# Optimization experiments

Measured on AMD Instinct MI355X. Metric: run time of the kernel, lower is better.

Reference implementation:

```python
import jax, jax.numpy as jnp
import numpy as np
import math

B, C, FDIM, TP = 32, 64, 128, 32
NHID, NOUT, E, RATIO = 256, 128, 512, 0.8
BN_EPS = 1e-5


def setup_inputs() -> dict:
    key = jax.random.key(0)
    ks = jax.random.split(key, 10)
    nrm = lambda k, shp, s=1.0: jax.random.normal(k, shp, jnp.float32) * s
    return {
        "h": nrm(ks[0], (B, C, FDIM, TP)),
        "edge_index": jax.random.randint(ks[1], (2, E), 0, C, dtype=jnp.int32),
        "edge_weight": jax.random.uniform(ks[2], (E,), jnp.float32),
        "gc1_w": nrm(ks[3], (FDIM, NHID), 1.0 / math.sqrt(FDIM)),
        "gc1_b": jnp.zeros((NHID,), jnp.float32),
        "bn1_gamma": jnp.ones((NHID,), jnp.float32),
        "bn1_beta": jnp.zeros((NHID,), jnp.float32),
        "bn1_mean": jnp.zeros((NHID,), jnp.float32),
        "bn1_var": jnp.ones((NHID,), jnp.float32),
        "prelu1_a": jnp.full((1,), 0.25, jnp.float32),
        "pool1_w": nrm(ks[4], (NHID, 1), 1.0 / math.sqrt(NHID)),
        "pool1_b": jnp.zeros((1,), jnp.float32),
        "gc2_w": nrm(ks[5], (NHID, NOUT), 1.0 / math.sqrt(NHID)),
        "gc2_b": jnp.zeros((NOUT,), jnp.float32),
        "bn2_gamma": jnp.ones((NOUT,), jnp.float32),
        "bn2_beta": jnp.zeros((NOUT,), jnp.float32),
        "bn2_mean": jnp.zeros((NOUT,), jnp.float32),
        "bn2_var": jnp.ones((NOUT,), jnp.float32),
        "prelu2_a": jnp.full((1,), 0.25, jnp.float32),
        "pool2_w": nrm(ks[6], (NOUT, 1), 1.0 / math.sqrt(NOUT)),
        "pool2_b": jnp.zeros((1,), jnp.float32),
    }


def _gcn(x, row, col, w, W, b, n):
    """PyG GCNConv: x @ W, add self-loops (weight 1), symmetric norm, scatter to col, + bias."""
    xw = x @ W
    loop = jnp.arange(n, dtype=row.dtype)
    r = jnp.concatenate([row, loop])
    c = jnp.concatenate([col, loop])
    wf = jnp.concatenate([w, jnp.ones((n,), x.dtype)])
    deg = jax.ops.segment_sum(wf, c, num_segments=n)
    deg_safe = jnp.where(deg > 0, deg, 1.0)
    dis = jnp.where(deg > 0, jax.lax.rsqrt(deg_safe), 0.0)  # deg^-1/2, inf -> 0
    norm = dis[r] * wf * dis[c]
    out = jax.ops.segment_sum(norm[:, None] * xw[r], c, num_segments=n)
    return out + b


def _bn(x, gamma, beta, mean, var):
    return gamma * (x - mean) * jax.lax.rsqrt(var + BN_EPS) + beta


def _prelu(x, a):
    return jnp.where(x >= 0, x, a * x)


def _sagpool(x, row, col, w, valid, Wp, bp, G, N, ratio):
    """SAGPool: GCN score (no edge weights => valid mask as binary weights), per-graph top-k,
    gate by tanh(score), reindex edges (filter_adj via masking). All graphs have N nodes."""
    n = G * N
    score = _gcn(x, row, col, valid.astype(x.dtype), Wp, bp, n)[:, 0]
    k = math.ceil(ratio * N)  # static: uniform graph sizes
    _, idx = jax.lax.top_k(score.reshape(G, N), k)
    perm = (jnp.arange(G, dtype=row.dtype)[:, None] * N + idx.astype(row.dtype)).reshape(-1)
    xk = x[perm] * jnp.tanh(score[perm])[:, None]
    node_map = jnp.full((n,), -1, dtype=row.dtype).at[perm].set(
        jnp.arange(G * k, dtype=row.dtype))
    nr, nc = node_map[row], node_map[col]
    v2 = valid & (nr >= 0) & (nc >= 0)
    nr = jnp.where(v2, nr, 0)
    nc = jnp.where(v2, nc, 0)
    w2 = jnp.where(v2, w, 0.0)
    return xk, nr, nc, w2, v2, k


def _forward(h, edge_index, edge_weight, gc1_w, gc1_b, bn1_gamma, bn1_beta, bn1_mean,
             bn1_var, prelu1_a, pool1_w, pool1_b, gc2_w, gc2_b, bn2_gamma, bn2_beta,
             bn2_mean, bn2_var, prelu2_a, pool2_w, pool2_b):
    b, c, f, tp = h.shape
    G = b * tp
    x = jnp.transpose(h, (0, 3, 1, 2)).reshape(G * c, f)  # fold time into batch of graphs
    offs = jnp.arange(G, dtype=edge_index.dtype) * c
    row = (edge_index[0][None, :] + offs[:, None]).reshape(-1)
    col = (edge_index[1][None, :] + offs[:, None]).reshape(-1)
    w = jnp.tile(edge_weight, G)
    valid = jnp.ones(row.shape, dtype=bool)

    x = _gcn(x, row, col, w, gc1_w, gc1_b, G * c)
    x = _prelu(_bn(x, bn1_gamma, bn1_beta, bn1_mean, bn1_var), prelu1_a)
    x, row, col, w, valid, k1 = _sagpool(x, row, col, w, valid, pool1_w, pool1_b, G, c, RATIO)
    # dropout: eval mode -> identity
    x = _gcn(x, row, col, w, gc2_w, gc2_b, G * k1)
    x = _prelu(_bn(x, bn2_gamma, bn2_beta, bn2_mean, bn2_var), prelu2_a)
    x, row, col, w, valid, k2 = _sagpool(x, row, col, w, valid, pool2_w, pool2_b, G, k1, RATIO)

    z = x.reshape(G, k2, -1).mean(axis=1)  # global_mean_pool (uniform segments)
    z_seq = z.reshape(b, tp, -1)
    return x, z_seq


def reference(h, edge_index, edge_weight, gc1_w, gc1_b, bn1_gamma, bn1_beta, bn1_mean,
              bn1_var, prelu1_a, pool1_w, pool1_b, gc2_w, gc2_b, bn2_gamma, bn2_beta,
              bn2_mean, bn2_var, prelu2_a, pool2_w, pool2_b):
    return _forward(h, edge_index, edge_weight, gc1_w, gc1_b, bn1_gamma, bn1_beta,
                    bn1_mean, bn1_var, prelu1_a, pool1_w, pool1_b, gc2_w, gc2_b,
                    bn2_gamma, bn2_beta, bn2_mean, bn2_var, prelu2_a, pool2_w, pool2_b)
```

## Files before the change

### kernel.cpp

```cpp
#include <hip/hip_runtime.h>
#include <math.h>

#define B_   32
#define C_   64
#define F_   128
#define TP_  32
#define G_   (B_*TP_)
#define NHID 256
#define NOUT 128
#define E_   512
#define K1_  52
#define K2_  42
#define N2_  (G_*K1_)

typedef __attribute__((ext_vector_type(8))) short short8_t;
typedef __attribute__((ext_vector_type(4))) float f32x4_t;

__device__ __forceinline__ void split_bf16(float v, unsigned short &h, unsigned short &l) {
  unsigned u = __float_as_uint(v);
  unsigned hb = (u + 0x7FFFu + ((u >> 16) & 1u)) & 0xFFFF0000u;
  float hf = __uint_as_float(hb);
  float r = v - hf;
  unsigned ur = __float_as_uint(r);
  unsigned lb = (ur + 0x7FFFu + ((ur >> 16) & 1u)) >> 16;
  h = (unsigned short)(hb >> 16);
  l = (unsigned short)lb;
}

__global__ __launch_bounds__(256) void build_A1(const int* __restrict__ ei,
                                                const float* __restrict__ ew,
                                                float* __restrict__ A1,
                                                float* __restrict__ As1) {
  __shared__ float A1s[C_*C_], As1s[C_*C_];
  __shared__ float dg[C_], dgs[C_], dis[C_], diss[C_];
  int t = threadIdx.x;
  for (int i = t; i < C_*C_; i += 256) { A1s[i] = 0.f; As1s[i] = 0.f; }
  if (t < C_) { dg[t] = 1.f; dgs[t] = 1.f; }
  int r0[2], c0[2]; float w0[2];
#pragma unroll
  for (int p = 0; p < 2; ++p) {
    int e = t + p*256;
    r0[p] = ei[e]; c0[p] = ei[E_ + e]; w0[p] = ew[e];
  }
  __syncthreads();
#pragma unroll
  for (int p = 0; p < 2; ++p) {
    atomicAdd(&dg[c0[p]], w0[p]);
    atomicAdd(&dgs[c0[p]], 1.f);
  }
  __syncthreads();
  if (t < C_) { dis[t] = rsqrtf(dg[t]); diss[t] = rsqrtf(dgs[t]); }
  __syncthreads();
#pragma unroll
  for (int p = 0; p < 2; ++p) {
    int r = r0[p], c = c0[p];
    atomicAdd(&A1s[c*C_ + r],  dis[r] * w0[p] * dis[c]);
    atomicAdd(&As1s[c*C_ + r], diss[r] * diss[c]);
  }
  if (t < C_) {
    atomicAdd(&A1s[t*C_ + t],  dis[t] * dis[t]);
    atomicAdd(&As1s[t*C_ + t], diss[t] * diss[t]);
  }
  __syncthreads();
  for (int i = t; i < C_*C_; i += 256) { A1[i] = A1s[i]; As1[i] = As1s[i]; }
}

__global__ __launch_bounds__(256) void w1prep(const float* __restrict__ W1,
                                              unsigned short* __restrict__ Whi,
                                              unsigned short* __restrict__ Wlo) {
  int tid = blockIdx.x*256 + threadIdx.x;
  int col = tid >> 6, k2 = tid & 63;
  float v0 = W1[(size_t)(2*k2)*NHID + col];
  float v1 = W1[(size_t)(2*k2+1)*NHID + col];
  unsigned short h0,l0,h1,l1;
  split_bf16(v0, h0, l0);
  split_bf16(v1, h1, l1);
  *(unsigned*)&Whi[(size_t)col*128 + 2*k2] = (unsigned)h0 | ((unsigned)h1 << 16);
  *(unsigned*)&Wlo[(size_t)col*128 + 2*k2] = (unsigned)l0 | ((unsigned)l1 << 16);
}

__global__ __launch_bounds__(256) void preagg_b(const float* __restrict__ h,
                                                const float* __restrict__ A1,
                                                float* __restrict__ xa2) {
  int bid = blockIdx.x; int b = bid >> 5, q = bid & 31;
  __shared__ float At[64*68];
  __shared__ __align__(16) float Hs[64*132];
  int t = threadIdx.x;
#pragma unroll
  for (int p = 0; p < 16; ++p) {
    int m = t + p*256;
    At[(m & 63)*68 + (m >> 6)] = A1[m];
  }
  const float* hb = h + ((size_t)b*64)*4096 + q*128;
#pragma unroll
  for (int p = 0; p < 8; ++p) {
    int idx = t + p*256;
    int j = idx >> 5, f4 = idx & 31;
    *(float4*)&Hs[j*132 + f4*4] = *(const float4*)(hb + (size_t)j*4096 + f4*4);
  }
  __syncthreads();
  int tx = t & 31, ty = t >> 5;
  float acc[8][4] = {};
  for (int j = 0; j < 64; ++j) {
    float a[8];
    *(float4*)&a[0] = *(const float4*)&At[j*68 + ty*8];
    *(float4*)&a[4] = *(const float4*)&At[j*68 + ty*8 + 4];
    float4 hv = *(const float4*)&Hs[j*132 + tx*4];
#pragma unroll
    for (int i = 0; i < 8; ++i) {
      acc[i][0] = fmaf(a[i], hv.x, acc[i][0]);
      acc[i][1] = fmaf(a[i], hv.y, acc[i][1]);
      acc[i][2] = fmaf(a[i], hv.z, acc[i][2]);
      acc[i][3] = fmaf(a[i], hv.w, acc[i][3]);
    }
  }
  float* outp = xa2 + (((size_t)b*64) << 12) + q*128 + tx*4;
#pragma unroll
  for (int i = 0; i < 8; ++i) {
    int c = ty*8 + i;
    *(float4*)(outp + ((size_t)c << 12)) =
        make_float4(acc[i][0], acc[i][1], acc[i][2], acc[i][3]);
  }
}

__global__ __launch_bounds__(256) void xa_cvt(const float* __restrict__ xa2,
                                              unsigned short* __restrict__ xahi,
                                              unsigned short* __restrict__ xalo) {
  int bid = blockIdx.x;
  int b = bid >> 5, c0 = (bid & 31) * 2;
  __shared__ float xs[8192];
  int t = threadIdx.x;
  const float* src = xa2 + ((size_t)(b*64 + c0) << 12);
#pragma unroll
  for (int p = 0; p < 8; ++p) {
    int idx = (t + p*256) * 4;
    *(float4*)&xs[idx] = *(const float4*)(src + idx);
  }
  __syncthreads();
  int row_l = t >> 2, fq = t & 3;
  int c_l = row_l >> 5, tp = row_l & 31;
  size_t R = ((size_t)b*32 + tp)*64 + c0 + c_l;
  const float* base = &xs[c_l*4096 + tp];
#pragma unroll
  for (int i = 0; i < 4; ++i) {
    int f8 = fq + 4*i;
    unsigned hp[4], lp[4];
#pragma unroll
    for (int jj = 0; jj < 4; ++jj) {
      unsigned short h0,l0,h1,l1;
      split_bf16(base[(f8*8 + 2*jj    )*32], h0, l0);
      split_bf16(base[(f8*8 + 2*jj + 1)*32], h1, l1);
      hp[jj] = (unsigned)h0 | ((unsigned)h1 << 16);
      lp[jj] = (unsigned)l0 | ((unsigned)l1 << 16);
    }
    *(uint4*)&xahi[R*128 + f8*8] = make_uint4(hp[0], hp[1], hp[2], hp[3]);
    *(uint4*)&xalo[R*128 + f8*8] = make_uint4(lp[0], lp[1], lp[2], lp[3]);
  }
}

__global__ __launch_bounds__(256) void gemm1m(const unsigned short* __restrict__ xahi,
                                              const unsigned short* __restrict__ xalo,
                                              const unsigned short* __restrict__ Whi,
                                              const unsigned short* __restrict__ Wlo,
                                              const float* __restrict__ gc1b,
                                              const float* __restrict__ g1,
                                              const float* __restrict__ be1,
                                              const float* __restrict__ mu1,
                                              const float* __restrict__ v1,
                                              const float* __restrict__ pa1,
                                              const float* __restrict__ pw1,
                                              float* __restrict__ y1,
                                              float* __restrict__ dots2) {
  __shared__ unsigned short Ahs[64*40], Als[64*40];
  __shared__ unsigned short Bhs[128*40], Bls[128*40];
  __shared__ float dsum[64*4];
  int t = threadIdx.x;
  int row0 = blockIdx.x * 64;
  int colhalf = blockIdx.y;
  int w = t >> 6, l = t & 63, lr = l & 15, lg = l >> 4;
  f32x4_t acc[4][2] = {};
  for (int k0 = 0; k0 < 128; k0 += 32) {
    {
      int row = t >> 2, kq = t & 3;
      size_t src = (size_t)(row0 + row)*128 + k0 + kq*8;
      *(uint4*)&Ahs[row*40 + kq*8] = *(const uint4*)&xahi[src];
      *(uint4*)&Als[row*40 + kq*8] = *(const uint4*)&xalo[src];
    }
#pragma unroll
    for (int p = 0; p < 2; ++p) {
      int id = t + p*256;
      int colb = id >> 2, kq = id & 3;
      size_t src = (size_t)(colhalf*128 + colb)*128 + k0 + kq*8;
      *(uint4*)&Bhs[colb*40 + kq*8] = *(const uint4*)&Whi[src];
      *(uint4*)&Bls[colb*40 + kq*8] = *(const uint4*)&Wlo[src];
    }
    __syncthreads();
    short8_t ah[4], al[4], bh[2], bl[2];
#pragma unroll
    for (int s = 0; s < 4; ++s) {
      int off = (s*16 + lr)*40 + lg*8;
      ah[s] = *(const short8_t*)&Ahs[off];
      al[s] = *(const short8_t*)&Als[off];
    }
#pragma unroll
    for (int t2 = 0; t2 < 2; ++t2) {
      int off = (w*32 + t2*16 + lr)*40 + lg*8;
      bh[t2] = *(const short8_t*)&Bhs[off];
      bl[t2] = *(const short8_t*)&Bls[off];
    }
#pragma unroll
    for (int s = 0; s < 4; ++s)
#pragma unroll
      for (int t2 = 0; t2 < 2; ++t2) {
        acc[s][t2] = __builtin_amdgcn_mfma_f32_16x16x32_bf16(ah[s], bh[t2], acc[s][t2], 0, 0, 0);
        acc[s][t2] = __builtin_amdgcn_mfma_f32_16x16x32_bf16(al[s], bh[t2], acc[s][t2], 0, 0, 0);
        acc[s][t2] = __builtin_amdgcn_mfma_f32_16x16x32_bf16(ah[s], bl[t2], acc[s][t2], 0, 0, 0);
      }
    __syncthreads();
  }
  float sc_[2], sh_[2], pw_[2];
#pragma unroll
  for (int t2 = 0; t2 < 2; ++t2) {
    int col_g = colhalf*128 + w*32 + t2*16 + lr;
    float s = g1[col_g] * rsqrtf(v1[col_g] + 1e-5f);
    sc_[t2] = s;
    sh_[t2] = (gc1b[col_g] - mu1[col_g])*s + be1[col_g];
    pw_[t2] = pw1[col_g];
  }
  float a1v = pa1[0];
#pragma unroll
  for (int s = 0; s < 4; ++s)
#pragma unroll
    for (int j = 0; j < 4; ++j) {
      int row_l = s*16 + lg*4 + j;
      size_t R = (size_t)row0 + row_l;
      float d = 0.f;
#pragma unroll
      for (int t2 = 0; t2 < 2; ++t2) {
        float o = acc[s][t2][j]*sc_[t2] + sh_[t2];
        o = o >= 0.f ? o : a1v*o;
        y1[R*NHID + colhalf*128 + w*32 + t2*16 + lr] = o;
        d += o * pw_[t2];
      }
      d += __shfl_xor(d, 1);
      d += __shfl_xor(d, 2);
      d += __shfl_xor(d, 4);
      d += __shfl_xor(d, 8);
      if (lr == 0) dsum[row_l*4 + w] = d;
    }
  __syncthreads();
  if (t < 64)
    dots2[((size_t)row0 + t)*2 + colhalf] =
        (dsum[t*4+0] + dsum[t*4+1]) + (dsum[t*4+2] + dsum[t*4+3]);
}

__global__ __launch_bounds__(256) void pool1s(const float* __restrict__ dots2,
                                              const float* __restrict__ As1,
                                              const float* __restrict__ p1b,
                                              int* __restrict__ rowsrc,
                                              float* __restrict__ rowgate,
                                              int* __restrict__ nidx) {
  int g = blockIdx.x, t = threadIdx.x;
  __shared__ float As1s[64*65];
  __shared__ float sp[64], s[64];
  __shared__ int perm[K1_];
  __shared__ float gate[K1_];
  for (int i = t; i < 4096; i += 256)
    As1s[(i >> 6)*65 + (i & 63)] = As1[i];
  if (t < 64) sp[t] = dots2[(g*64 + t)*2] + dots2[(g*64 + t)*2 + 1];
  __syncthreads();
  if (t < 64) {
    float acc = p1b[0];
    for (int j = 0; j < 64; ++j) acc = fmaf(As1s[t*65 + j], sp[j], acc);
    s[t] = acc;
  }
  __syncthreads();
  if (t < 64) {
    float si = s[t];
    int rank = 0;
    for (int j = 0; j < 64; ++j) {
      float sj = s[j];
      rank += (sj > si) || (sj == si && j < t);
    }
    nidx[g*64 + t] = (rank < K1_) ? rank : -1;
    if (rank < K1_) { perm[rank] = t; gate[rank] = tanhf(si); }
  }
  __syncthreads();
  if (t < K1_) {
    rowsrc[g*K1_ + t]  = g*64 + perm[t];
    rowgate[g*K1_ + t] = gate[t];
  }
}

__global__ __launch_bounds__(256) void gemm2g(const float* __restrict__ y1,
                                              const int* __restrict__ rowsrc,
                                              const float* __restrict__ rowgate,
                                              const float* __restrict__ W2,
                                              float* __restrict__ xw2) {
  __shared__ __align__(16) float As[16][132];
  __shared__ __align__(16) float Bs[16][132];
  int t = threadIdx.x;
  int row0 = blockIdx.x * 128;
  int tx = t & 15, ty = t >> 4;
  float acc[8][8] = {};
  for (int k0 = 0; k0 < NHID; k0 += 16) {
#pragma unroll
    for (int p = 0; p < 2; ++p) {
      int rm = (t >> 2) + p*64, tq = t & 3;
      int sr = rowsrc[row0 + rm];
      float gt = rowgate[row0 + rm];
      float4 av = *(const float4*)(y1 + (size_t)sr * NHID + k0 + 4*tq);
      As[4*tq+0][rm] = av.x * gt; As[4*tq+1][rm] = av.y * gt;
      As[4*tq+2][rm] = av.z * gt; As[4*tq+3][rm] = av.w * gt;
    }
#pragma unroll
    for (int p = 0; p < 2; ++p) {
      int rk = (t >> 5) + p*8, cn = (t & 31)*4;
      *(float4*)&Bs[rk][cn] = *(const float4*)(W2 + (size_t)(k0 + rk)*NOUT + cn);
    }
    __syncthreads();
#pragma unroll
    for (int kk = 0; kk < 16; ++kk) {
      float a[8], b[8];
      *(float4*)&a[0] = *(const float4*)&As[kk][4*ty];
      *(float4*)&a[4] = *(const float4*)&As[kk][64 + 4*ty];
      *(float4*)&b[0] = *(const float4*)&Bs[kk][4*tx];
      *(float4*)&b[4] = *(const float4*)&Bs[kk][64 + 4*tx];
#pragma unroll
      for (int i = 0; i < 8; ++i)
#pragma unroll
        for (int j = 0; j < 8; ++j)
          acc[i][j] = fmaf(a[i], b[j], acc[i][j]);
    }
    __syncthreads();
  }
#pragma unroll
  for (int ih = 0; ih < 2; ++ih)
#pragma unroll
    for (int i = 0; i < 4; ++i) {
      int r = row0 + ih*64 + 4*ty + i;
#pragma unroll
      for (int jh = 0; jh < 2; ++jh) {
        float4 v = make_float4(acc[ih*4+i][jh*4+0], acc[ih*4+i][jh*4+1],
                               acc[ih*4+i][jh*4+2], acc[ih*4+i][jh*4+3]);
        *(float4*)(xw2 + (size_t)r * NOUT + jh*64 + 4*tx) = v;
      }
    }
}

__global__ __launch_bounds__(256) void mega2r(const int* __restrict__ ei,
                                              const float* __restrict__ ew,
                                              const int* __restrict__ nidx,
                                              const float* __restrict__ xw2,
                                              const float* __restrict__ gc2b,
                                              const float* __restrict__ g2,
                                              const float* __restrict__ be2,
                                              const float* __restrict__ mu2,
                                              const float* __restrict__ v2,
                                              const float* __restrict__ pa2,
                                              const float* __restrict__ pw2,
                                              const float* __restrict__ p2b,
                                              float* __restrict__ out) {
  int g = blockIdx.x, t = threadIdx.x;
  __shared__ float A2t[64*68];
  __shared__ float As2s[K1_*K1_];
  __shared__ __align__(16) float xs[K1_*132];
  __shared__ float dg[K1_], dgs[K1_], dis[K1_], diss[K1_], d[K1_], s[K1_], gA[K1_];
  __shared__ int nm[C_], rankA[K1_];
  __shared__ float4 zpart[8][32];

  for (int i = t; i < 64*68; i += 256) A2t[i] = 0.f;
  for (int i = t; i < K1_*K1_; i += 256) As2s[i] = 0.f;
  if (t < C_) nm[t] = nidx[g*C_ + t];
  if (t < K1_) { dg[t] = 1.f; dgs[t] = 1.f; }
  for (int p = 0; p < 7; ++p) {
    int idx = t + p*256;
    if (idx < K1_*32) {
      int r = idx >> 5, f4 = idx & 31;
      *(float4*)&xs[r*132 + f4*4] =
          *(const float4*)(xw2 + ((size_t)g*K1_ + r)*NOUT + f4*4);
    }
  }
  int eR[2], eC[2]; float eW[2];
#pragma unroll
  for (int p = 0; p < 2; ++p) {
    int e = t + p*256;
    eR[p] = ei[e]; eC[p] = ei[E_ + e]; eW[p] = ew[e];
  }
  __syncthreads();
  int nr[2], nc[2]; bool val[2];
#pragma unroll
  for (int p = 0; p < 2; ++p) {
    nr[p] = nm[eR[p]]; nc[p] = nm[eC[p]];
    val[p] = (nr[p] >= 0) && (nc[p] >= 0);
    if (val[p]) { atomicAdd(&dg[nc[p]], eW[p]); atomicAdd(&dgs[nc[p]], 1.f); }
  }
  __syncthreads();
  if (t < K1_) { dis[t] = rsqrtf(dg[t]); diss[t] = rsqrtf(dgs[t]); }
  __syncthreads();
#pragma unroll
  for (int p = 0; p < 2; ++p) {
    if (val[p]) {
      atomicAdd(&A2t[nr[p]*68 + nc[p]],  dis[nr[p]] * eW[p] * dis[nc[p]]);
      atomicAdd(&As2s[nc[p]*K1_ + nr[p]], diss[nr[p]] * diss[nc[p]]);
    }
  }
  if (t < K1_) {
    atomicAdd(&A2t[t*68 + t],   dis[t]*dis[t]);
    atomicAdd(&As2s[t*K1_ + t], diss[t]*diss[t]);
  }
  __syncthreads();
  int tx = t & 31, ty = t >> 5;
  float4 scv, shv, pwv;
  {
    int col = 4*tx;
    float4 gv = *(const float4*)(g2 + col);
    float4 vv = *(const float4*)(v2 + col);
    float4 bv = *(const float4*)(be2 + col);
    float4 mv = *(const float4*)(mu2 + col);
    float4 b0 = *(const float4*)(gc2b + col);
    scv.x = gv.x * rsqrtf(vv.x + 1e-5f); scv.y = gv.y * rsqrtf(vv.y + 1e-5f);
    scv.z = gv.z * rsqrtf(vv.z + 1e-5f); scv.w = gv.w * rsqrtf(vv.w + 1e-5f);
    shv = make_float4((b0.x - mv.x)*scv.x + bv.x, (b0.y - mv.y)*scv.y + bv.y,
                      (b0.z - mv.z)*scv.z + bv.z, (b0.w - mv.w)*scv.w + bv.w);
    pwv = *(const float4*)(pw2 + col);
  }
  float a2v = pa2[0];
  float acc[8][4] = {};
  for (int j = 0; j < K1_; ++j) {
    float a[8];
    *(float4*)&a[0] = *(const float4*)&A2t[j*68 + ty*8];
    *(float4*)&a[4] = *(const float4*)&A2t[j*68 + ty*8 + 4];
    float4 xv = *(const float4*)&xs[j*132 + tx*4];
#pragma unroll
    for (int i = 0; i < 8; ++i) {
      acc[i][0] = fmaf(a[i], xv.x, acc[i][0]);
      acc[i][1] = fmaf(a[i], xv.y, acc[i][1]);
      acc[i][2] = fmaf(a[i], xv.z, acc[i][2]);
      acc[i][3] = fmaf(a[i], xv.w, acc[i][3]);
    }
  }
#pragma unroll
  for (int i = 0; i < 8; ++i) {
    int c = ty*8 + i;
    if (c < K1_) {
      float4 o;
      o.x = acc[i][0]*scv.x + shv.x; o.y = acc[i][1]*scv.y + shv.y;
      o.z = acc[i][2]*scv.z + shv.z; o.w = acc[i][3]*scv.w + shv.w;
      o.x = o.x >= 0.f ? o.x : a2v*o.x; o.y = o.y >= 0.f ? o.y : a2v*o.y;
      o.z = o.z >= 0.f ? o.z : a2v*o.z; o.w = o.w >= 0.f ? o.w : a2v*o.w;
      acc[i][0] = o.x; acc[i][1] = o.y; acc[i][2] = o.z; acc[i][3] = o.w;
      float dp = o.x*pwv.x + o.y*pwv.y + o.z*pwv.z + o.w*pwv.w;
      dp += __shfl_xor(dp, 1);
      dp += __shfl_xor(dp, 2);
      dp += __shfl_xor(dp, 4);
      dp += __shfl_xor(dp, 8);
      dp += __shfl_xor(dp, 16);
      if (tx == 0) d[c] = dp;
    }
  }
  __syncthreads();
  if (t < K1_) {
    float sv = p2b[0];
    for (int j = 0; j < K1_; ++j) sv = fmaf(As2s[t*K1_ + j], d[j], sv);
    s[t] = sv;
  }
  __syncthreads();
  if (t < K1_) {
    float si = s[t];
    int rank = 0;
    for (int j = 0; j < K1_; ++j) {
      float sj = s[j];
      rank += (sj > si) || (sj == si && j < t);
    }
    rankA[t] = rank;
    gA[t] = tanhf(si);
  }
  __syncthreads();
  float4 zp = make_float4(0.f, 0.f, 0.f, 0.f);
#pragma unroll
  for (int i = 0; i < 8; ++i) {
    int c = ty*8 + i;
    if (c < K1_) {
      int r = rankA[c];
      if (r < K2_) {
        float gt = gA[c];
        float4 v = make_float4(acc[i][0]*gt, acc[i][1]*gt, acc[i][2]*gt, acc[i][3]*gt);
        *(float4*)(out + ((size_t)g*K2_ + r)*NOUT + 4*tx) = v;
        zp.x += v.x; zp.y += v.y; zp.z += v.z; zp.w += v.w;
      }
    }
  }
  zpart[ty][tx] = zp;
  __syncthreads();
  if (t < 32) {
    float4 z = make_float4(0.f, 0.f, 0.f, 0.f);
#pragma unroll
    for (int k = 0; k < 8; ++k) {
      float4 v = zpart[k][t];
      z.x += v.x; z.y += v.y; z.z += v.z; z.w += v.w;
    }
    const float inv = 1.0f / (float)K2_;
    z.x *= inv; z.y *= inv; z.z *= inv; z.w *= inv;
    *(float4*)(out + (size_t)G_*K2_*NOUT + (size_t)g*NOUT + 4*t) = z;
  }
}

extern "C" void kernel_launch(void* const* d_in, const int* in_sizes, int n_in,
                              void* d_out, int out_size, void* d_ws, size_t ws_size,
                              hipStream_t stream) {
  const float* h    = (const float*)d_in[0];
  const int*   ei   = (const int*)  d_in[1];
  const float* ew   = (const float*)d_in[2];
  const float* gc1w = (const float*)d_in[3];
  const float* gc1b = (const float*)d_in[4];
  const float* bn1g = (const float*)d_in[5];
  const float* bn1b = (const float*)d_in[6];
  const float* bn1m = (const float*)d_in[7];
  const float* bn1v = (const float*)d_in[8];
  const float* pr1a = (const float*)d_in[9];
  const float* p1w  = (const float*)d_in[10];
  const float* p1b  = (const float*)d_in[11];
  const float* gc2w = (const float*)d_in[12];
  const float* gc2b = (const float*)d_in[13];
  const float* bn2g = (const float*)d_in[14];
  const float* bn2b = (const float*)d_in[15];
  const float* bn2m = (const float*)d_in[16];
  const float* bn2v = (const float*)d_in[17];
  const float* pr2a = (const float*)d_in[18];
  const float* p2w  = (const float*)d_in[19];
  const float* p2b  = (const float*)d_in[20];

  float* w = (float*)d_ws;
  float*          A1      = w;
  float*          As1     = w + 4096;
  float*          dots2   = w + 8192;
  int*            nidx    = (int*)(w + 139264);
  int*            rowsrc  = (int*)(w + 204800);
  float*          rowgate = w + 258048;
  unsigned short* W1thi   = (unsigned short*)(w + 311296);
  unsigned short* W1tlo   = (unsigned short*)(w + 327680);
  float*          xa2     = w + 344064;
  float*          y1      = w + 8732672;
  unsigned short* xahi    = (unsigned short*)(w + 25509888);
  unsigned short* xalo    = (unsigned short*)(w + 29704192);
  float*          xw2     = xa2;

  build_A1<<<1, 256, 0, stream>>>(ei, ew, A1, As1);
  w1prep<<<64, 256, 0, stream>>>(gc1w, W1thi, W1tlo);
  preagg_b<<<1024, 256, 0, stream>>>(h, A1, xa2);
  xa_cvt<<<1024, 256, 0, stream>>>(xa2, xahi, xalo);
  gemm1m<<<dim3(1024, 2), 256, 0, stream>>>(xahi, xalo, W1thi, W1tlo, gc1b,
                                            bn1g, bn1b, bn1m, bn1v, pr1a, p1w,
                                            y1, dots2);
  pool1s<<<G_, 256, 0, stream>>>(dots2, As1, p1b, rowsrc, rowgate, nidx);
  gemm2g<<<416, 256, 0, stream>>>(y1, rowsrc, rowgate, gc2w, xw2);
  mega2r<<<G_, 256, 0, stream>>>(ei, ew, nidx, xw2, gc2b, bn2g, bn2b, bn2m, bn2v,
                                 pr2a, p2w, p2b, (float*)d_out);
}
```

Measured before the change: 165.5 us.

## Run second GCN GEMM on bf16x3 MFMA and move gate scaling downstream

Replaces the FP32 SIMT gathered GEMM for the second GCN layer with a bf16 MFMA GEMM. Both operands are split into three bf16 parts and combined with six MFMA products per tile to keep near-FP32 accuracy. The first GEMM now writes y1 as three bf16 planes instead of fp32, W2 gets a split-and-transpose prep kernel, and the per-row tanh gate is applied when mega2r loads xw2, which is valid because the gate is a per-row scalar. It adds one launch and six times the matrix-unit work, and the split epilogue in gemm1m costs more ALU work and more stores (three 2-byte writes versus one 4-byte write).

Result: faster. 155.1 us (-6.3%).

```diff
diff --git a/kernel.cpp b/kernel.cpp
--- a/kernel.cpp
+++ b/kernel.cpp
@@ -24,6 +24,23 @@
   unsigned ur = __float_as_uint(r);
   unsigned lb = (ur + 0x7FFFu + ((ur >> 16) & 1u)) >> 16;
   h = (unsigned short)(hb >> 16);
+  l = (unsigned short)lb;
+}
+
+__device__ __forceinline__ void split3_bf16(float v, unsigned short &h,
+                                            unsigned short &m, unsigned short &l) {
+  unsigned u = __float_as_uint(v);
+  unsigned hb = (u + 0x7FFFu + ((u >> 16) & 1u)) & 0xFFFF0000u;
+  float hf = __uint_as_float(hb);
+  float r1 = v - hf;
+  unsigned u1 = __float_as_uint(r1);
+  unsigned mb = (u1 + 0x7FFFu + ((u1 >> 16) & 1u)) & 0xFFFF0000u;
+  float mf = __uint_as_float(mb);
+  float r2 = r1 - mf;
+  unsigned u2 = __float_as_uint(r2);
+  unsigned lb = (u2 + 0x7FFFu + ((u2 >> 16) & 1u)) >> 16;
+  h = (unsigned short)(hb >> 16);
+  m = (unsigned short)(mb >> 16);
   l = (unsigned short)lb;
 }
 
@@ -79,6 +96,22 @@
   *(unsigned*)&Wlo[(size_t)col*128 + 2*k2] = (unsigned)l0 | ((unsigned)l1 << 16);
 }
 
+__global__ __launch_bounds__(256) void w2prep(const float* __restrict__ W2,
+                                              unsigned short* __restrict__ Whi,
+                                              unsigned short* __restrict__ Wmid,
+                                              unsigned short* __restrict__ Wlo) {
+  int tid = blockIdx.x*256 + threadIdx.x;
+  int col = tid >> 7, k2 = tid & 127;
+  float v0 = W2[(size_t)(2*k2)*NOUT + col];
+  float v1 = W2[(size_t)(2*k2+1)*NOUT + col];
+  unsigned short h0,m0,l0,h1,m1,l1;
+  split3_bf16(v0, h0, m0, l0);
+  split3_bf16(v1, h1, m1, l1);
+  *(unsigned*)&Whi [(size_t)col*256 + 2*k2] = (unsigned)h0 | ((unsigned)h1 << 16);
+  *(unsigned*)&Wmid[(size_t)col*256 + 2*k2] = (unsigned)m0 | ((unsigned)m1 << 16);
+  *(unsigned*)&Wlo [(size_t)col*256 + 2*k2] = (unsigned)l0 | ((unsigned)l1 << 16);
+}
+
 __global__ __launch_bounds__(256) void preagg_b(const float* __restrict__ h,
                                                 const float* __restrict__ A1,
                                                 float* __restrict__ xa2) {
@@ -169,7 +202,9 @@
                                               const float* __restrict__ v1,
                                               const float* __restrict__ pa1,
                                               const float* __restrict__ pw1,
-                                              float* __restrict__ y1,
+                                              unsigned short* __restrict__ y1hi,
+                                              unsigned short* __restrict__ y1mid,
+                                              unsigned short* __restrict__ y1lo,
                                               float* __restrict__ dots2) {
   __shared__ unsigned short Ahs[64*40], Als[64*40];
   __shared__ unsigned short Bhs[128*40], Bls[128*40];
@@ -239,7 +274,12 @@
       for (int t2 = 0; t2 < 2; ++t2) {
         float o = acc[s][t2][j]*sc_[t2] + sh_[t2];
         o = o >= 0.f ? o : a1v*o;
-        y1[R*NHID + colhalf*128 + w*32 + t2*16 + lr] = o;
+        unsigned short hh, mm, ll;
+        split3_bf16(o, hh, mm, ll);
+        size_t oi = R*NHID + colhalf*128 + w*32 + t2*16 + lr;
+        y1hi[oi]  = hh;
+        y1mid[oi] = mm;
+        y1lo[oi]  = ll;
         d += o * pw_[t2];
       }
       d += __shfl_xor(d, 1);
@@ -292,66 +332,84 @@
   }
 }
 
-__global__ __launch_bounds__(256) void gemm2g(const float* __restrict__ y1,
+__global__ __launch_bounds__(256) void gemm2m(const unsigned short* __restrict__ y1hi,
+                                              const unsigned short* __restrict__ y1mid,
+                                              const unsigned short* __restrict__ y1lo,
                                               const int* __restrict__ rowsrc,
-                                              const float* __restrict__ rowgate,
-                                              const float* __restrict__ W2,
+                                              const unsigned short* __restrict__ Whi,
+                                              const unsigned short* __restrict__ Wmid,
+                                              const unsigned short* __restrict__ Wlo,
                                               float* __restrict__ xw2) {
-  __shared__ __align__(16) float As[16][132];
-  __shared__ __align__(16) float Bs[16][132];
+  __shared__ unsigned short Ahs[64*40], Ams[64*40], Als[64*40];
+  __shared__ unsigned short Bhs[128*40], Bms[128*40], Bls[128*40];
   int t = threadIdx.x;
-  int row0 = blockIdx.x * 128;
-  int tx = t & 15, ty = t >> 4;
-  float acc[8][8] = {};
-  for (int k0 = 0; k0 < NHID; k0 += 16) {
+  int row0 = blockIdx.x * 64;
+  int w = t >> 6, l = t & 63, lr = l & 15, lg = l >> 4;
+  int arow = t >> 2, akq = t & 3;
+  size_t asrc = (size_t)rowsrc[row0 + arow] * NHID;
+  f32x4_t acc[4][2] = {};
+  for (int k0 = 0; k0 < NHID; k0 += 32) {
+    {
+      size_t src = asrc + k0 + akq*8;
+      *(uint4*)&Ahs[arow*40 + akq*8] = *(const uint4*)&y1hi[src];
+      *(uint4*)&Ams[arow*40 + akq*8] = *(const uint4*)&y1mid[src];
+      *(uint4*)&Als[arow*40 + akq*8] = *(const uint4*)&y1lo[src];
+    }
 #pragma unroll
     for (int p = 0; p < 2; ++p) {
-      int rm = (t >> 2) + p*64, tq = t & 3;
-      int sr = rowsrc[row0 + rm];
-      float gt = rowgate[row0 + rm];
-      float4 av = *(const float4*)(y1 + (size_t)sr * NHID + k0 + 4*tq);
-      As[4*tq+0][rm] = av.x * gt; As[4*tq+1][rm] = av.y * gt;
-      As[4*tq+2][rm] = av.z * gt; As[4*tq+3][rm] = av.w * gt;
-    }
-#pragma unroll
-    for (int p = 0; p < 2; ++p) {
-      int rk = (t >> 5) + p*8, cn = (t & 31)*4;
-      *(float4*)&Bs[rk][cn] = *(const float4*)(W2 + (size_t)(k0 + rk)*NOUT + cn);
+      int id = t + p*256;
+      int colb = id >> 2, kq = id & 3;
+      size_t src = (size_t)colb*256 + k0 + kq*8;
+      *(uint4*)&Bhs[colb*40 + kq*8] = *(const uint4*)&Whi[src];
+      *(uint4*)&Bms[colb*40 + kq*8] = *(const uint4*)&Wmid[src];
+      *(uint4*)&Bls[colb*40 + kq*8] = *(const uint4*)&Wlo[src];
     }
     __syncthreads();
-#pragma unroll
-    for (int kk = 0; kk < 16; ++kk) {
-      float a[8], b[8];
-      *(float4*)&a[0] = *(const float4*)&As[kk][4*ty];
-      *(float4*)&a[4] = *(const float4*)&As[kk][64 + 4*ty];
-      *(float4*)&b[0] = *(const float4*)&Bs[kk][4*tx];
-      *(float4*)&b[4] = *(const float4*)&Bs[kk][64 + 4*tx];
-#pragma unroll
-      for (int i = 0; i < 8; ++i)
-#pragma unroll
-        for (int j = 0; j < 8; ++j)
-          acc[i][j] = fmaf(a[i], b[j], acc[i][j]);
-    }
+    short8_t ah[4], am[4], al[4], bh[2], bm[2], bl[2];
+#pragma unroll
+    for (int s = 0; s < 4; ++s) {
+      int off = (s*16 + lr)*40 + lg*8;
+      ah[s] = *(const short8_t*)&Ahs[off];
+      am[s] = *(const short8_t*)&Ams[off];
+      al[s] = *(const short8_t*)&Als[off];
+    }
+#pragma unroll
+    for (int t2 = 0; t2 < 2; ++t2) {
+      int off = (w*32 + t2*16 + lr)*40 + lg*8;
+      bh[t2] = *(const short8_t*)&Bhs[off];
+      bm[t2] = *(const short8_t*)&Bms[off];
+      bl[t2] = *(const short8_t*)&Bls[off];
+    }
+#pragma unroll
+    for (int s = 0; s < 4; ++s)
+#pragma unroll
+      for (int t2 = 0; t2 < 2; ++t2) {
+        acc[s][t2] = __builtin_amdgcn_mfma_f32_16x16x32_bf16(ah[s], bh[t2], acc[s][t2], 0, 0, 0);
+        acc[s][t2] = __builtin_amdgcn_mfma_f32_16x16x32_bf16(ah[s], bm[t2], acc[s][t2], 0, 0, 0);
+        acc[s][t2] = __builtin_amdgcn_mfma_f32_16x16x32_bf16(am[s], bh[t2], acc[s][t2], 0, 0, 0);
+        acc[s][t2] = __builtin_amdgcn_mfma_f32_16x16x32_bf16(ah[s], bl[t2], acc[s][t2], 0, 0, 0);
+        acc[s][t2] = __builtin_amdgcn_mfma_f32_16x16x32_bf16(am[s], bm[t2], acc[s][t2], 0, 0, 0);
+        acc[s][t2] = __builtin_amdgcn_mfma_f32_16x16x32_bf16(al[s], bh[t2], acc[s][t2], 0, 0, 0);
+      }
     __syncthreads();
   }
 #pragma unroll
-  for (int ih = 0; ih < 2; ++ih)
-#pragma unroll
-    for (int i = 0; i < 4; ++i) {
-      int r = row0 + ih*64 + 4*ty + i;
-#pragma unroll
-      for (int jh = 0; jh < 2; ++jh) {
-        float4 v = make_float4(acc[ih*4+i][jh*4+0], acc[ih*4+i][jh*4+1],
-                               acc[ih*4+i][jh*4+2], acc[ih*4+i][jh*4+3]);
-        *(float4*)(xw2 + (size_t)r * NOUT + jh*64 + 4*tx) = v;
+  for (int s = 0; s < 4; ++s)
+#pragma unroll
+    for (int t2 = 0; t2 < 2; ++t2)
+#pragma unroll
+      for (int j = 0; j < 4; ++j) {
+        int row_l = s*16 + lg*4 + j;
+        int col = w*32 + t2*16 + lr;
+        xw2[(size_t)(row0 + row_l)*NOUT + col] = acc[s][t2][j];
       }
-    }
 }
 
 __global__ __launch_bounds__(256) void mega2r(const int* __restrict__ ei,
                                               const float* __restrict__ ew,
                                               const int* __restrict__ nidx,
                                               const float* __restrict__ xw2,
+                                              const float* __restrict__ rowgate,
                                               const float* __restrict__ gc2b,
                                               const float* __restrict__ g2,
                                               const float* __restrict__ be2,
@@ -377,8 +435,10 @@
     int idx = t + p*256;
     if (idx < K1_*32) {
       int r = idx >> 5, f4 = idx & 31;
-      *(float4*)&xs[r*132 + f4*4] =
-          *(const float4*)(xw2 + ((size_t)g*K1_ + r)*NOUT + f4*4);
+      float gt = rowgate[g*K1_ + r];
+      float4 v = *(const float4*)(xw2 + ((size_t)g*K1_ + r)*NOUT + f4*4);
+      v.x *= gt; v.y *= gt; v.z *= gt; v.w *= gt;
+      *(float4*)&xs[r*132 + f4*4] = v;
     }
   }
   int eR[2], eC[2]; float eW[2];
@@ -540,21 +600,27 @@
   float*          rowgate = w + 258048;
   unsigned short* W1thi   = (unsigned short*)(w + 311296);
   unsigned short* W1tlo   = (unsigned short*)(w + 327680);
-  float*          xa2     = w + 344064;
-  float*          y1      = w + 8732672;
-  unsigned short* xahi    = (unsigned short*)(w + 25509888);
-  unsigned short* xalo    = (unsigned short*)(w + 29704192);
+  unsigned short* W2thi   = (unsigned short*)(w + 344064);
+  unsigned short* W2tmid  = (unsigned short*)(w + 360448);
+  unsigned short* W2tlo   = (unsigned short*)(w + 376832);
+  float*          xa2     = w + 393216;
+  unsigned short* xahi    = (unsigned short*)(w + 8781824);
+  unsigned short* xalo    = (unsigned short*)(w + 12976128);
+  unsigned short* y1hi    = (unsigned short*)(w + 17170432);
+  unsigned short* y1mid   = (unsigned short*)(w + 25559040);
+  unsigned short* y1lo    = (unsigned short*)(w + 33947648);
   float*          xw2     = xa2;
 
   build_A1<<<1, 256, 0, stream>>>(ei, ew, A1, As1);
   w1prep<<<64, 256, 0, stream>>>(gc1w, W1thi, W1tlo);
+  w2prep<<<64, 256, 0, stream>>>(gc2w, W2thi, W2tmid, W2tlo);
   preagg_b<<<1024, 256, 0, stream>>>(h, A1, xa2);
   xa_cvt<<<1024, 256, 0, stream>>>(xa2, xahi, xalo);
   gemm1m<<<dim3(1024, 2), 256, 0, stream>>>(xahi, xalo, W1thi, W1tlo, gc1b,
                                             bn1g, bn1b, bn1m, bn1v, pr1a, p1w,
-                                            y1, dots2);
+                                            y1hi, y1mid, y1lo, dots2);
   pool1s<<<G_, 256, 0, stream>>>(dots2, As1, p1b, rowsrc, rowgate, nidx);
-  gemm2g<<<416, 256, 0, stream>>>(y1, rowsrc, rowgate, gc2w, xw2);
-  mega2r<<<G_, 256, 0, stream>>>(ei, ew, nidx, xw2, gc2b, bn2g, bn2b, bn2m, bn2v,
-                                 pr2a, p2w, p2b, (float*)d_out);
-}
+  gemm2m<<<832, 256, 0, stream>>>(y1hi, y1mid, y1lo, rowsrc, W2thi, W2tmid, W2tlo, xw2);
+  mega2r<<<G_, 256, 0, stream>>>(ei, ew, nidx, xw2, rowgate, gc2b, bn2g, bn2b,
+                                 bn2m, bn2v, pr2a, p2w, p2b, (float*)d_out);
+}
```
